# Kernel tuning notes

Hardware: AMD Instinct MI355X
Metric: run time of the kernel (lower is better)

The kernel has to match this reference:

```python
import jax, jax.numpy as jnp
import numpy as np


def setup_inputs() -> dict:
    key = jax.random.key(0)
    ks = jax.random.split(key, 5)
    T, B, E = 2048, 2, 1024
    return {
        "query": jax.random.normal(ks[0], (T, B, E), dtype=jnp.float32),
        "in_proj_weight": jax.random.normal(ks[1], (3 * E, E), dtype=jnp.float32) * (E ** -0.5),
        "in_proj_bias": jax.random.normal(ks[2], (3 * E,), dtype=jnp.float32) * 0.02,
        "out_proj_weight": jax.random.normal(ks[3], (E, E), dtype=jnp.float32) * (E ** -0.5),
        "out_proj_bias": jax.random.normal(ks[4], (E,), dtype=jnp.float32) * 0.02,
        "num_heads": 16,
    }


def reference(query, in_proj_weight, in_proj_bias, out_proj_weight, out_proj_bias, num_heads):
    T, B, E = query.shape
    H = num_heads
    d = E // H
    scaling = d ** -0.5
    # fused QKV projection: (T,B,E) @ (E,3E) + bias -> (T,B,3E)
    qkv = jnp.einsum('tbe,fe->tbf', query, in_proj_weight) + in_proj_bias
    # torch views (T*B, 3E) as (T, B*H, 3, d): per token layout is (H, 3, d)
    qkv = qkv.reshape(T, B, H, 3, d)
    q = qkv[..., 0, :] * scaling  # (T,B,H,d)
    k = qkv[..., 1, :]
    v = qkv[..., 2, :]
    scores = jnp.einsum('tbhd,sbhd->bhts', q, k)  # (B,H,T,T)
    probs = jax.nn.softmax(scores.astype(jnp.float32), axis=-1).astype(scores.dtype)
    ctx = jnp.einsum('bhts,sbhd->tbhd', probs, v).reshape(T, B, E)
    out = jnp.einsum('tbe,fe->tbf', ctx, out_proj_weight) + out_proj_bias
    return out
```

## Files before the change

kernel.cpp:

```cpp
#include <hip/hip_runtime.h>
#include <hip/hip_bf16.h>
#include <math.h>

constexpr int T_DIM = 2048;
constexpr int B_DIM = 2;
constexpr int E_DIM = 1024;
constexpr float QK_SCALE = 0.18033688011112042f;

#if __has_builtin(__builtin_amdgcn_exp2f)
#define EXP2F(x) __builtin_amdgcn_exp2f(x)
#else
#define EXP2F(x) exp2f(x)
#endif

typedef __attribute__((ext_vector_type(8))) short short8;
typedef __attribute__((ext_vector_type(4))) float f32x4;

__device__ inline short f2bf(float x) {
    union { __hip_bfloat16 b; short s; } u;
    u.b = __float2bfloat16(x);
    return u.s;
}
__device__ inline float bf2f(short s) {
    union { __hip_bfloat16 b; short s; } u;
    u.s = s;
    return __bfloat162float(u.b);
}

__device__ inline int pack_bf16(float hi, float lo) {
    union { float f; unsigned u; } a, b;
    a.f = hi; b.f = lo;
    return (int)__builtin_amdgcn_perm(a.u + 0x8000u, b.u + 0x8000u, 0x07060302u);
}

__device__ inline void gl2lds16(const void* g, void* l) {
    __builtin_amdgcn_global_load_lds(
        (const __attribute__((address_space(1))) unsigned int*)g,
        (__attribute__((address_space(3))) unsigned int*)l, 16, 0, 0);
}

__device__ inline f32x4 mfma_bf16(short8 a, short8 b, f32x4 c) {
    return __builtin_amdgcn_mfma_f32_16x16x32_bf16(a, b, c, 0, 0, 0);
}

__global__ __launch_bounds__(256)
void split_all_kernel(const float* __restrict__ query,
                      const float* __restrict__ w_in,
                      const float* __restrict__ w_out,
                      short* __restrict__ qh,
                      short* __restrict__ wih, short* __restrict__ wil,
                      short* __restrict__ woh, short* __restrict__ wol,
                      int nq4, int nwi4, int nwo4)
{
    int i = blockIdx.x * 256 + threadIdx.x;
    const float* src; short* dh; short* dl; int k; int do_lo;
    if (i < nq4) { src = query; dh = qh; dl = nullptr; k = i; do_lo = 0; }
    else if (i < nq4 + nwi4) { src = w_in; dh = wih; dl = wil; k = i - nq4; do_lo = 1; }
    else { src = w_out; dh = woh; dl = wol; k = i - nq4 - nwi4; do_lo = 1; }
    float4 v = ((const float4*)src)[k];
    short h0 = f2bf(v.x), h1 = f2bf(v.y), h2 = f2bf(v.z), h3 = f2bf(v.w);
    ((short4*)dh)[k] = make_short4(h0, h1, h2, h3);
    if (do_lo) {
        short l0 = f2bf(v.x - bf2f(h0));
        short l1 = f2bf(v.y - bf2f(h1));
        short l2 = f2bf(v.z - bf2f(h2));
        short l3 = f2bf(v.w - bf2f(h3));
        ((short4*)dl)[k] = make_short4(l0, l1, l2, l3);
    }
}

__global__ __launch_bounds__(256)
void gemm_in(const short* __restrict__ Ah,
             const short* __restrict__ Wh, const short* __restrict__ Wl,
             const float* __restrict__ bias,
             short* __restrict__ qkv, short* __restrict__ kp,
             short* __restrict__ vtp,
             int M, int N, int K)
{
    __shared__ __align__(16) short AsH[128 * 64];
    __shared__ __align__(16) short WsH[128 * 64];
    __shared__ __align__(16) short WsL[128 * 64];

    const int tid  = threadIdx.x;
    const int lane = tid & 63;
    const int wave = tid >> 6;
    const int rm = (wave >> 1) * 64;
    const int cn = (wave & 1) * 64;
    const int m0 = blockIdx.y * 128;
    const int n0 = blockIdx.x * 128;

    const int srow = wave * 32 + (lane >> 3);
    const int swz  = (lane & 7) ^ (lane >> 3);
    const size_t gaB = (size_t)(m0 + srow) * K + swz * 8;
    const size_t gwB = (size_t)(n0 + srow) * K + swz * 8;
    const size_t rowK8 = (size_t)8 * K;

    const f32x4 zero = {0.f, 0.f, 0.f, 0.f};
    f32x4 acc[4][4];
    #pragma unroll
    for (int i = 0; i < 4; ++i)
        #pragma unroll
        for (int j = 0; j < 4; ++j) acc[i][j] = zero;

    const int fr = lane & 15;
    const int qc = lane >> 4;

    for (int k0 = 0; k0 < K; k0 += 64) {
        if (k0) __syncthreads();
        #pragma unroll
        for (int c = 0; c < 4; ++c) {
            gl2lds16(Ah + gaB + k0 + c * rowK8, &AsH[(wave * 32 + c * 8) * 64]);
            gl2lds16(Wh + gwB + k0 + c * rowK8, &WsH[(wave * 32 + c * 8) * 64]);
            gl2lds16(Wl + gwB + k0 + c * rowK8, &WsL[(wave * 32 + c * 8) * 64]);
        }
        __syncthreads();

        #pragma unroll
        for (int kk = 0; kk < 2; ++kk) {
            short8 ahf[4], bhf[4], blf[4];
            #pragma unroll
            for (int i = 0; i < 4; ++i) {
                int r = rm + 16 * i + fr;
                int slot = (4 * kk + qc) ^ (r & 7);
                ahf[i] = *(const short8*)&AsH[r * 64 + slot * 8];
            }
            #pragma unroll
            for (int j = 0; j < 4; ++j) {
                int r = cn + 16 * j + fr;
                int slot = (4 * kk + qc) ^ (r & 7);
                bhf[j] = *(const short8*)&WsH[r * 64 + slot * 8];
                blf[j] = *(const short8*)&WsL[r * 64 + slot * 8];
            }
            #pragma unroll
            for (int i = 0; i < 4; ++i)
                #pragma unroll
                for (int j = 0; j < 4; ++j) {
                    acc[i][j] = mfma_bf16(ahf[i], bhf[j], acc[i][j]);
                    acc[i][j] = mfma_bf16(ahf[i], blf[j], acc[i][j]);
                }
        }
    }

    const int g = lane >> 4;
    #pragma unroll
    for (int j = 0; j < 4; ++j) {
        const int colu = n0 + cn + 16 * j;
        const int col  = colu + fr;
        const float bj = bias[col];
        const int c6  = colu >> 6;
        const int grp = c6 % 3;
        const int h   = c6 / 3;
        const int d   = (colu & 63) + fr;
        if (grp == 0) {
            #pragma unroll
            for (int i = 0; i < 4; ++i)
                #pragma unroll
                for (int r = 0; r < 4; ++r) {
                    int row = m0 + rm + 16 * i + g * 4 + r;
                    qkv[(size_t)row * 3072 + col] =
                        f2bf((acc[i][j][r] + bj) * QK_SCALE);
                }
        } else if (grp == 1) {
            const int hh = d >> 5, gk = (d >> 3) & 3, ii = d & 7;
            #pragma unroll
            for (int i = 0; i < 4; ++i)
                #pragma unroll
                for (int r = 0; r < 4; ++r) {
                    int row = m0 + rm + 16 * i + g * 4 + r;
                    int t = row >> 1, bb = row & 1;
                    int m = t & 63;
                    int R = (m & 32) | ((m & 24) >> 1) | ((m & 4) << 2) | (m & 3);
                    size_t off = (size_t)(bb * 16 + h) * 131072
                               + (size_t)(t >> 6) * 4096
                               + (size_t)(((2 * (R >> 4) + hh) * 64
                                           + gk * 16 + (R & 15)) * 8 + ii);
                    kp[off] = f2bf(acc[i][j][r] + bj);
                }
        } else {
            const int jd = d >> 4, frv = d & 15;
            #pragma unroll
            for (int i = 0; i < 4; ++i)
                #pragma unroll
                for (int r = 0; r < 4; ++r) {
                    int row = m0 + rm + 16 * i + g * 4 + r;
                    int t = row >> 1, bb = row & 1;
                    int tl = t & 63;
                    size_t off = (size_t)(bb * 16 + h) * 131072
                               + (size_t)(t >> 6) * 4096
                               + (size_t)(((2 * jd + (tl >> 5)) * 64
                                           + ((tl >> 3) & 3) * 16 + frv) * 8
                                          + (tl & 7));
                    vtp[off] = f2bf(acc[i][j][r] + bj);
                }
        }
    }
}

__global__ __launch_bounds__(256)
void gemm_out(const short* __restrict__ Ah, const short* __restrict__ Al,
              const short* __restrict__ Wh, const short* __restrict__ Wl,
              const float* __restrict__ bias, float* __restrict__ Cout,
              int M, int N, int K)
{
    __shared__ __align__(16) short AsH[64 * 64];
    __shared__ __align__(16) short AsL[64 * 64];
    __shared__ __align__(16) short WsH[128 * 64];
    __shared__ __align__(16) short WsL[128 * 64];

    const int tid  = threadIdx.x;
    const int lane = tid & 63;
    const int wave = tid >> 6;
    const int m0 = blockIdx.y * 64;
    const int n0 = blockIdx.x * 128;

    const int sarow = wave * 16 + (lane >> 3);
    const int swrow = wave * 32 + (lane >> 3);
    const int swz   = (lane & 7) ^ (lane >> 3);
    const size_t gaB = (size_t)(m0 + sarow) * K + swz * 8;
    const size_t gwB = (size_t)(n0 + swrow) * K + swz * 8;
    const size_t rowK8 = (size_t)8 * K;

    const f32x4 zero = {0.f, 0.f, 0.f, 0.f};
    f32x4 acc[4][2];
    #pragma unroll
    for (int i = 0; i < 4; ++i) { acc[i][0] = zero; acc[i][1] = zero; }

    const int fr = lane & 15;
    const int g = lane >> 4;

    for (int k0 = 0; k0 < K; k0 += 64) {
        if (k0) __syncthreads();
        #pragma unroll
        for (int c = 0; c < 2; ++c) {
            gl2lds16(Ah + gaB + k0 + c * rowK8, &AsH[(wave * 16 + c * 8) * 64]);
            gl2lds16(Al + gaB + k0 + c * rowK8, &AsL[(wave * 16 + c * 8) * 64]);
        }
        #pragma unroll
        for (int c = 0; c < 4; ++c) {
            gl2lds16(Wh + gwB + k0 + c * rowK8, &WsH[(wave * 32 + c * 8) * 64]);
            gl2lds16(Wl + gwB + k0 + c * rowK8, &WsL[(wave * 32 + c * 8) * 64]);
        }
        __syncthreads();

        #pragma unroll
        for (int kk = 0; kk < 2; ++kk) {
            short8 ahf[4], alf[4], bhf[2], blf[2];
            #pragma unroll
            for (int i = 0; i < 4; ++i) {
                int r = 16 * i + fr;
                int slot = (4 * kk + g) ^ (r & 7);
                ahf[i] = *(const short8*)&AsH[r * 64 + slot * 8];
                alf[i] = *(const short8*)&AsL[r * 64 + slot * 8];
            }
            #pragma unroll
            for (int j = 0; j < 2; ++j) {
                int r = wave * 32 + 16 * j + fr;
                int slot = (4 * kk + g) ^ (r & 7);
                bhf[j] = *(const short8*)&WsH[r * 64 + slot * 8];
                blf[j] = *(const short8*)&WsL[r * 64 + slot * 8];
            }
            #pragma unroll
            for (int i = 0; i < 4; ++i)
                #pragma unroll
                for (int j = 0; j < 2; ++j) {
                    acc[i][j] = mfma_bf16(ahf[i], bhf[j], acc[i][j]);
                    acc[i][j] = mfma_bf16(ahf[i], blf[j], acc[i][j]);
                    acc[i][j] = mfma_bf16(alf[i], bhf[j], acc[i][j]);
                }
        }
    }

    #pragma unroll
    for (int j = 0; j < 2; ++j) {
        int col = n0 + wave * 32 + 16 * j + fr;
        float bj = bias[col];
        #pragma unroll
        for (int i = 0; i < 4; ++i)
            #pragma unroll
            for (int r = 0; r < 4; ++r) {
                int row = m0 + 16 * i + g * 4 + r;
                Cout[(size_t)row * N + col] = acc[i][j][r] + bj;
            }
    }
}

__global__ __launch_bounds__(512, 2)
void attn_mfma(const short* __restrict__ qkv, const short* __restrict__ kp,
               const short* __restrict__ vtp,
               short* __restrict__ ctxh, short* __restrict__ ctxl)
{
    __shared__ __align__(16) char ldsRaw[256 * 68 * 4 + 1024];
    short (*ldsKV)[2][8192] = (short (*)[2][8192])ldsRaw;

    const int tid  = threadIdx.x;
    const int lane = tid & 63;
    const int wave = tid >> 6;
    const int w4    = wave & 3;
    const int khalf = wave >> 2;
    const int fr = lane & 15;
    const int g  = lane >> 4;

    const int id = blockIdx.x;
    const int x = id & 7, y = id >> 3;
    const int bh = x * 4 + (y & 3);
    const int q0 = (y >> 2) * 256;
    const int b = bh >> 4, h = bh & 15;

    short8 aq[4][2];
    #pragma unroll
    for (int set = 0; set < 4; ++set) {
        const short* qrow = qkv +
            ((size_t)(q0 + w4 * 64 + set * 16 + fr) * 2 + b) * 3072 + h * 192;
        aq[set][0] = *(const short8*)(qrow + g * 8);
        aq[set][1] = *(const short8*)(qrow + 32 + g * 8);
    }

    const short* kt = kp  + (size_t)bh * 131072 + (size_t)khalf * 16 * 4096;
    const short* vt = vtp + (size_t)bh * 131072 + (size_t)khalf * 16 * 4096;

    short8 ONES;
    #pragma unroll
    for (int i = 0; i < 8; ++i) ONES[i] = (short)0x3F80;

    const f32x4 zero = {0.f, 0.f, 0.f, 0.f};
    f32x4 o[4][4];
    #pragma unroll
    for (int set = 0; set < 4; ++set)
        #pragma unroll
        for (int jd = 0; jd < 4; ++jd) o[set][jd] = zero;
    f32x4 lacc[4] = {zero, zero, zero, zero};

    auto stage = [&](int it, int sel) {
        const short* ks = kt + it * 4096 + w4 * 1024 + lane * 8;
        const short* vs = vt + it * 4096 + w4 * 1024 + lane * 8;
        short* base = &ldsKV[khalf][sel][0];
        gl2lds16(ks,       base + w4 * 1024);
        gl2lds16(ks + 512, base + w4 * 1024 + 512);
        gl2lds16(vs,       base + 4096 + w4 * 1024);
        gl2lds16(vs + 512, base + 4096 + w4 * 1024 + 512);
    };

    stage(0, 0);
    #pragma unroll 2
    for (int it = 0; it < 16; ++it) {
        const int cur = it & 1;
        __syncthreads();
        if (it + 1 < 16) stage(it + 1, cur ^ 1);
        const short* Kb = &ldsKV[khalf][cur][0];
        const short* Vb = Kb + 4096;

        union { int w[4]; short8 v; } A0[4];
        #pragma unroll
        for (int s = 0; s < 2; ++s) {
            short8 k0 = *(const short8*)&Kb[(2 * s) * 512 + lane * 8];
            short8 k1 = *(const short8*)&Kb[(2 * s + 1) * 512 + lane * 8];
            #pragma unroll
            for (int set = 0; set < 4; ++set) {
                f32x4 a = zero;
                a = mfma_bf16(k0, aq[set][0], a);
                a = mfma_bf16(k1, aq[set][1], a);
                float e0 = EXP2F(a[0]), e1 = EXP2F(a[1]);
                float e2 = EXP2F(a[2]), e3 = EXP2F(a[3]);
                A0[set].w[s * 2]     = pack_bf16(e1, e0);
                A0[set].w[s * 2 + 1] = pack_bf16(e3, e2);
            }
        }
        #pragma unroll
        for (int set = 0; set < 4; ++set)
            lacc[set] = mfma_bf16(A0[set].v, ONES, lacc[set]);
        #pragma unroll
        for (int jd = 0; jd < 4; ++jd) {
            short8 v0 = *(const short8*)&Vb[(2 * jd) * 512 + lane * 8];
            #pragma unroll
            for (int set = 0; set < 4; ++set)
                o[set][jd] = mfma_bf16(A0[set].v, v0, o[set][jd]);
        }

        union { int w[4]; short8 v; } A1[4];
        #pragma unroll
        for (int s = 0; s < 2; ++s) {
            short8 k0 = *(const short8*)&Kb[(2 * s + 4) * 512 + lane * 8];
            short8 k1 = *(const short8*)&Kb[(2 * s + 5) * 512 + lane * 8];
            #pragma unroll
            for (int set = 0; set < 4; ++set) {
                f32x4 a = zero;
                a = mfma_bf16(k0, aq[set][0], a);
                a = mfma_bf16(k1, aq[set][1], a);
                float e0 = EXP2F(a[0]), e1 = EXP2F(a[1]);
                float e2 = EXP2F(a[2]), e3 = EXP2F(a[3]);
                A1[set].w[s * 2]     = pack_bf16(e1, e0);
                A1[set].w[s * 2 + 1] = pack_bf16(e3, e2);
            }
        }
        #pragma unroll
        for (int set = 0; set < 4; ++set)
            lacc[set] = mfma_bf16(A1[set].v, ONES, lacc[set]);
        #pragma unroll
        for (int jd = 0; jd < 4; ++jd) {
            short8 v1 = *(const short8*)&Vb[(2 * jd + 1) * 512 + lane * 8];
            #pragma unroll
            for (int set = 0; set < 4; ++set)
                o[set][jd] = mfma_bf16(A1[set].v, v1, o[set][jd]);
        }
    }

    __syncthreads();
    float* oshare = (float*)ldsRaw;
    float* lshare = oshare + 256 * 68;

    if (khalf == 1) {
        #pragma unroll
        for (int set = 0; set < 4; ++set)
            #pragma unroll
            for (int r = 0; r < 4; ++r) {
                int row = w4 * 64 + set * 16 + 4 * g + r;
                #pragma unroll
                for (int jd = 0; jd < 4; ++jd)
                    oshare[row * 68 + 16 * jd + fr] = o[set][jd][r];
                if (fr == 0) lshare[row] = lacc[set][r];
            }
    }
    __syncthreads();
    if (khalf == 0) {
        #pragma unroll
        for (int set = 0; set < 4; ++set)
            #pragma unroll
            for (int r = 0; r < 4; ++r) {
                int row = w4 * 64 + set * 16 + 4 * g + r;
                float lt = lacc[set][r] + lshare[row];
                float inv = 1.f / lt;
                int t = q0 + row;
                size_t base = ((size_t)t * B_DIM + b) * E_DIM + h * 64;
                #pragma unroll
                for (int jd = 0; jd < 4; ++jd) {
                    float v = (o[set][jd][r] + oshare[row * 68 + 16 * jd + fr]) * inv;
                    short hs = f2bf(v);
                    short ls = f2bf(v - bf2f(hs));
                    ctxh[base + 16 * jd + fr] = hs;
                    ctxl[base + 16 * jd + fr] = ls;
                }
            }
    }
}

extern "C" void kernel_launch(void* const* d_in, const int* in_sizes, int n_in,
                              void* d_out, int out_size, void* d_ws, size_t ws_size,
                              hipStream_t stream)
{
    const float* query = (const float*)d_in[0];
    const float* w_in  = (const float*)d_in[1];
    const float* b_in  = (const float*)d_in[2];
    const float* w_out = (const float*)d_in[3];
    const float* b_out = (const float*)d_in[4];
    float* out = (float*)d_out;

    char* ws = (char*)d_ws;
    short* qkv  = (short*)(ws);
    short* qh   = (short*)(ws + 25165824);
    short* wih  = (short*)(ws + 33554432);
    short* wil  = (short*)(ws + 39845888);
    short* woh  = (short*)(ws + 46137344);
    short* wol  = (short*)(ws + 48234496);
    short* vtp  = (short*)(ws + 50331648);
    short* kp   = (short*)(ws + 58720256);
    short* ctxh = (short*)(ws + 25165824);
    short* ctxl = (short*)(ws + 33554432);

    const int M = T_DIM * B_DIM;

    int nq4  = (M * E_DIM) / 4;
    int nwi4 = (3 * E_DIM * E_DIM) / 4;
    int nwo4 = (E_DIM * E_DIM) / 4;
    split_all_kernel<<<(nq4 + nwi4 + nwo4) / 256, 256, 0, stream>>>(
        query, w_in, w_out, qh, wih, wil, woh, wol, nq4, nwi4, nwo4);

    gemm_in<<<dim3(3 * E_DIM / 128, M / 128), 256, 0, stream>>>(
        qh, wih, wil, b_in, qkv, kp, vtp, M, 3 * E_DIM, E_DIM);

    attn_mfma<<<dim3(256), 512, 0, stream>>>(qkv, kp, vtp, ctxh, ctxl);

    gemm_out<<<dim3(E_DIM / 128, M / 64), 256, 0, stream>>>(
        ctxh, ctxl, woh, wol, b_out, out, M, E_DIM, E_DIM);
}
```

Before: 204.3 us.

## Split attention keys four ways with 128-query blocks and doubled grid

Each attention block now handles 128 queries instead of 256, and its 8 waves split the key range into four quarters, each with two query groups, instead of two halves. The grid doubles to 512 blocks, so more CUs are filled and per-block LDS use shrinks. Each iteration processes 32 keys per quarter, using half-tiles of the K/V layout. The partial sums are reduced serially through LDS in three stages. The cost is more K/V reloading across blocks (twice as many query tiles per head) and extra barriers in the reduction.

```diff
diff --git a/kernel.cpp b/kernel.cpp
--- a/kernel.cpp
+++ b/kernel.cpp
@@ -289,34 +289,33 @@
                const short* __restrict__ vtp,
                short* __restrict__ ctxh, short* __restrict__ ctxl)
 {
-    __shared__ __align__(16) char ldsRaw[256 * 68 * 4 + 1024];
-    short (*ldsKV)[2][8192] = (short (*)[2][8192])ldsRaw;
+    __shared__ __align__(16) short ldsKV[4][2][4096];
 
     const int tid  = threadIdx.x;
     const int lane = tid & 63;
     const int wave = tid >> 6;
-    const int w4    = wave & 3;
-    const int khalf = wave >> 2;
+    const int quarter = wave >> 1;
+    const int qg      = wave & 1;
     const int fr = lane & 15;
     const int g  = lane >> 4;
 
     const int id = blockIdx.x;
     const int x = id & 7, y = id >> 3;
     const int bh = x * 4 + (y & 3);
-    const int q0 = (y >> 2) * 256;
+    const int q0 = (y >> 2) * 128;
     const int b = bh >> 4, h = bh & 15;
 
     short8 aq[4][2];
     #pragma unroll
     for (int set = 0; set < 4; ++set) {
         const short* qrow = qkv +
-            ((size_t)(q0 + w4 * 64 + set * 16 + fr) * 2 + b) * 3072 + h * 192;
+            ((size_t)(q0 + qg * 64 + set * 16 + fr) * 2 + b) * 3072 + h * 192;
         aq[set][0] = *(const short8*)(qrow + g * 8);
         aq[set][1] = *(const short8*)(qrow + 32 + g * 8);
     }
 
-    const short* kt = kp  + (size_t)bh * 131072 + (size_t)khalf * 16 * 4096;
-    const short* vt = vtp + (size_t)bh * 131072 + (size_t)khalf * 16 * 4096;
+    const short* kt = kp  + (size_t)bh * 131072;
+    const short* vt = vtp + (size_t)bh * 131072;
 
     short8 ONES;
     #pragma unroll
@@ -331,13 +330,17 @@
     f32x4 lacc[4] = {zero, zero, zero, zero};
 
     auto stage = [&](int it, int sel) {
-        const short* ks = kt + it * 4096 + w4 * 1024 + lane * 8;
-        const short* vs = vt + it * 4096 + w4 * 1024 + lane * 8;
-        short* base = &ldsKV[khalf][sel][0];
-        gl2lds16(ks,       base + w4 * 1024);
-        gl2lds16(ks + 512, base + w4 * 1024 + 512);
-        gl2lds16(vs,       base + 4096 + w4 * 1024);
-        gl2lds16(vs + 512, base + 4096 + w4 * 1024 + 512);
+        const int ts = quarter * 16 + it;
+        const int t64 = ts >> 1, half = ts & 1;
+        const short* ksrc = kt + t64 * 4096 + half * 2048 + qg * 1024 + lane * 8;
+        short* kdst = &ldsKV[quarter][sel][qg * 1024];
+        gl2lds16(ksrc,       kdst);
+        gl2lds16(ksrc + 512, kdst + 512);
+        const short* vsrc = kt == nullptr ? nullptr : vt + t64 * 4096 + half * 512
+                          + (2 * qg) * 1024 + lane * 8;
+        short* vdst = &ldsKV[quarter][sel][2048 + (2 * qg) * 512];
+        gl2lds16(vsrc,        vdst);
+        gl2lds16(vsrc + 1024, vdst + 512);
     };
 
     stage(0, 0);
@@ -346,8 +349,8 @@
         const int cur = it & 1;
         __syncthreads();
         if (it + 1 < 16) stage(it + 1, cur ^ 1);
-        const short* Kb = &ldsKV[khalf][cur][0];
-        const short* Vb = Kb + 4096;
+        const short* Kb = &ldsKV[quarter][cur][0];
+        const short* Vb = Kb + 2048;
 
         union { int w[4]; short8 v; } A0[4];
         #pragma unroll
@@ -370,50 +373,23 @@
             lacc[set] = mfma_bf16(A0[set].v, ONES, lacc[set]);
         #pragma unroll
         for (int jd = 0; jd < 4; ++jd) {
-            short8 v0 = *(const short8*)&Vb[(2 * jd) * 512 + lane * 8];
+            short8 v0 = *(const short8*)&Vb[jd * 512 + lane * 8];
             #pragma unroll
             for (int set = 0; set < 4; ++set)
                 o[set][jd] = mfma_bf16(A0[set].v, v0, o[set][jd]);
         }
-
-        union { int w[4]; short8 v; } A1[4];
-        #pragma unroll
-        for (int s = 0; s < 2; ++s) {
-            short8 k0 = *(const short8*)&Kb[(2 * s + 4) * 512 + lane * 8];
-            short8 k1 = *(const short8*)&Kb[(2 * s + 5) * 512 + lane * 8];
-            #pragma unroll
-            for (int set = 0; set < 4; ++set) {
-                f32x4 a = zero;
-                a = mfma_bf16(k0, aq[set][0], a);
-                a = mfma_bf16(k1, aq[set][1], a);
-                float e0 = EXP2F(a[0]), e1 = EXP2F(a[1]);
-                float e2 = EXP2F(a[2]), e3 = EXP2F(a[3]);
-                A1[set].w[s * 2]     = pack_bf16(e1, e0);
-                A1[set].w[s * 2 + 1] = pack_bf16(e3, e2);
-            }
-        }
+    }
+
+    __syncthreads();
+    float* oshare = (float*)&ldsKV[0][0][0];
+    float* lshare = oshare + 128 * 68;
+
+    if (quarter == 1) {
         #pragma unroll
         for (int set = 0; set < 4; ++set)
-            lacc[set] = mfma_bf16(A1[set].v, ONES, lacc[set]);
-        #pragma unroll
-        for (int jd = 0; jd < 4; ++jd) {
-            short8 v1 = *(const short8*)&Vb[(2 * jd + 1) * 512 + lane * 8];
-            #pragma unroll
-            for (int set = 0; set < 4; ++set)
-                o[set][jd] = mfma_bf16(A1[set].v, v1, o[set][jd]);
-        }
-    }
-
-    __syncthreads();
-    float* oshare = (float*)ldsRaw;
-    float* lshare = oshare + 256 * 68;
-
-    if (khalf == 1) {
-        #pragma unroll
-        for (int set = 0; set < 4; ++set)
             #pragma unroll
             for (int r = 0; r < 4; ++r) {
-                int row = w4 * 64 + set * 16 + 4 * g + r;
+                int row = qg * 64 + set * 16 + 4 * g + r;
                 #pragma unroll
                 for (int jd = 0; jd < 4; ++jd)
                     oshare[row * 68 + 16 * jd + fr] = o[set][jd][r];
@@ -421,12 +397,38 @@
             }
     }
     __syncthreads();
-    if (khalf == 0) {
+    if (quarter == 2) {
         #pragma unroll
         for (int set = 0; set < 4; ++set)
             #pragma unroll
             for (int r = 0; r < 4; ++r) {
-                int row = w4 * 64 + set * 16 + 4 * g + r;
+                int row = qg * 64 + set * 16 + 4 * g + r;
+                #pragma unroll
+                for (int jd = 0; jd < 4; ++jd)
+                    oshare[row * 68 + 16 * jd + fr] += o[set][jd][r];
+                if (fr == 0) lshare[row] += lacc[set][r];
+            }
+    }
+    __syncthreads();
+    if (quarter == 3) {
+        #pragma unroll
+        for (int set = 0; set < 4; ++set)
+            #pragma unroll
+            for (int r = 0; r < 4; ++r) {
+                int row = qg * 64 + set * 16 + 4 * g + r;
+                #pragma unroll
+                for (int jd = 0; jd < 4; ++jd)
+                    oshare[row * 68 + 16 * jd + fr] += o[set][jd][r];
+                if (fr == 0) lshare[row] += lacc[set][r];
+            }
+    }
+    __syncthreads();
+    if (quarter == 0) {
+        #pragma unroll
+        for (int set = 0; set < 4; ++set)
+            #pragma unroll
+            for (int r = 0; r < 4; ++r) {
+                int row = qg * 64 + set * 16 + 4 * g + r;
                 float lt = lacc[set][r] + lshare[row];
                 float inv = 1.f / lt;
                 int t = q0 + row;
@@ -477,7 +479,7 @@
     gemm_in<<<dim3(3 * E_DIM / 128, M / 128), 256, 0, stream>>>(
         qh, wih, wil, b_in, qkv, kp, vtp, M, 3 * E_DIM, E_DIM);
 
-    attn_mfma<<<dim3(256), 512, 0, stream>>>(qkv, kp, vtp, ctxh, ctxl);
+    attn_mfma<<<dim3(512), 512, 0, stream>>>(qkv, kp, vtp, ctxh, ctxl);
 
     gemm_out<<<dim3(E_DIM / 128, M / 64), 256, 0, stream>>>(
         ctxh, ctxl, woh, wol, b_out, out, M, E_DIM, E_DIM);
```

Result: slower. 213.6 us (+4.6%).
